# Performance work log

Hardware: AMD Instinct MI355X
Metric: run time of the kernel (lower is better)

Reference implementation:

```python
import jax, jax.numpy as jnp
import numpy as np
import math

D_K = 64

def setup_inputs() -> dict:
    key = jax.random.key(0)
    k1, k2, k3, k4 = jax.random.split(key, 4)
    BH, S, dk = 32, 2048, D_K
    q = jax.random.normal(k1, (BH, S, dk), dtype=jnp.float32)
    k = jax.random.normal(k2, (BH, S, dk), dtype=jnp.float32)
    v = jax.random.normal(k3, (BH, S, dk), dtype=jnp.float32)
    mask = jax.random.uniform(k4, (BH, S, S), dtype=jnp.float32)
    return {"q": q, "k": k, "v": v, "mask": mask}

def reference(q, k, v, mask):
    # scores: [BH, S, S]
    scores = jnp.einsum('bqd,bkd->bqk', q, k) * (1.0 / math.sqrt(D_K))
    masked = scores * mask  # multiplicative mask before softmax
    attn = jax.nn.softmax(masked, axis=-1)
    return jnp.einsum('bqk,bkd->bqd', attn, v)
```

## Files before the change

### kernel.cpp

```cpp
#include <hip/hip_runtime.h>
#include <hip/hip_bf16.h>

#define BH    32
#define SEQ   2048
#define DK    64
#define QBLK  256
#define KBLK  64
#define NIT   (SEQ / KBLK)
#define KSTR  72

typedef short  short8  __attribute__((ext_vector_type(8)));
typedef float  f32x4   __attribute__((ext_vector_type(4)));
typedef float  float4v __attribute__((ext_vector_type(4)));
typedef unsigned short ushort4v __attribute__((ext_vector_type(4)));

__device__ __forceinline__ unsigned short f2bf(float f) {
    unsigned int u = __builtin_bit_cast(unsigned int, f);
    u += 0x7FFFu + ((u >> 16) & 1u);
    return (unsigned short)(u >> 16);
}

#if __has_builtin(__builtin_amdgcn_exp2f)
#define EXP2F(x) __builtin_amdgcn_exp2f(x)
#else
#define EXP2F(x) exp2f(x)
#endif

__global__ __launch_bounds__(1024, 4)
void sdpa_kernel(const float* __restrict__ Q, const float* __restrict__ K,
                 const float* __restrict__ V, const float* __restrict__ M,
                 float* __restrict__ O)
{
    __shared__ unsigned short sK [2][KBLK][KSTR];
    __shared__ unsigned short sVt[2][DK][KSTR];
    __shared__ unsigned short sP [16][16][KSTR];

    const int tid  = threadIdx.x;
    const int wave = tid >> 6;
    const int lane = tid & 63;
    const int g    = lane >> 4;
    const int li   = lane & 15;

    const int b  = blockIdx.x;
    const int qb = blockIdx.y * QBLK;

    const float* Kb = K + (size_t)b * SEQ * DK;
    const float* Vb = V + (size_t)b * SEQ * DK;

    const float QSC = 0.125f * 1.44269504f;
    short8 aq[2];
    {
        const size_t qoff = ((size_t)b * SEQ + (qb + wave * 16 + li)) * DK;
        #pragma unroll
        for (int kk = 0; kk < 2; ++kk) {
            const float* qp = Q + qoff + kk * 32 + g * 8;
            float4v q0 = *(const float4v*)(qp);
            float4v q1 = *(const float4v*)(qp + 4);
            #pragma unroll
            for (int i = 0; i < 4; ++i) {
                aq[kk][i]     = (short)f2bf(q0[i] * QSC);
                aq[kk][i + 4] = (short)f2bf(q1[i] * QSC);
            }
        }
    }

    const int sr = tid >> 4;
    const int sc = (tid & 15) * 4;
    const int vd = tid & 63;
    const int vk = (tid >> 6) * 4;

    const float* kp = Kb + (size_t)sr * DK + sc;
    const float* vp = Vb + (size_t)vk * DK + vd;
    const float* mbase = M + ((size_t)b * SEQ + (qb + wave * 16 + g * 4)) * SEQ + li;

    float4v kreg = *(const float4v*)kp;
    float vreg0 = vp[0 * DK], vreg1 = vp[1 * DK], vreg2 = vp[2 * DK], vreg3 = vp[3 * DK];
    {
        ushort4v pk;
        pk[0] = f2bf(kreg[0]); pk[1] = f2bf(kreg[1]);
        pk[2] = f2bf(kreg[2]); pk[3] = f2bf(kreg[3]);
        *(ushort4v*)(&sK[0][sr][sc]) = pk;
        ushort4v pv_;
        pv_[0] = f2bf(vreg0); pv_[1] = f2bf(vreg1);
        pv_[2] = f2bf(vreg2); pv_[3] = f2bf(vreg3);
        *(ushort4v*)(&sVt[0][vd][vk]) = pv_;
    }
    kp += KBLK * DK;  vp += KBLK * DK;
    kreg = *(const float4v*)kp;
    vreg0 = vp[0 * DK]; vreg1 = vp[1 * DK]; vreg2 = vp[2 * DK]; vreg3 = vp[3 * DK];

    float mkA[4][4], mkB[4][4];
    #pragma unroll
    for (int r = 0; r < 4; ++r) {
        #pragma unroll
        for (int t = 0; t < 4; ++t)
            mkA[r][t] = mbase[(size_t)r * SEQ + t * 16];
    }

    __syncthreads();

    f32x4 oacc[4] = {};
    float lsum[4] = {0.f, 0.f, 0.f, 0.f};

#define SDPA_BODY(IT, CUR, MKC, MKN)                                          \
    {                                                                         \
        if ((IT) + 1 < NIT) {                                                 \
            const float* mp = mbase + (size_t)((IT) + 1) * KBLK;              \
            _Pragma("unroll")                                                 \
            for (int r = 0; r < 4; ++r) {                                     \
                _Pragma("unroll")                                             \
                for (int t = 0; t < 4; ++t)                                   \
                    MKN[r][t] = mp[(size_t)r * SEQ + t * 16];                 \
            }                                                                 \
            ushort4v pk;                                                      \
            pk[0] = f2bf(kreg[0]); pk[1] = f2bf(kreg[1]);                     \
            pk[2] = f2bf(kreg[2]); pk[3] = f2bf(kreg[3]);                     \
            *(ushort4v*)(&sK[(CUR) ^ 1][sr][sc]) = pk;                        \
            ushort4v pv_;                                                     \
            pv_[0] = f2bf(vreg0); pv_[1] = f2bf(vreg1);                       \
            pv_[2] = f2bf(vreg2); pv_[3] = f2bf(vreg3);                       \
            *(ushort4v*)(&sVt[(CUR) ^ 1][vd][vk]) = pv_;                      \
            if ((IT) + 2 < NIT) {                                             \
                kp += KBLK * DK;  vp += KBLK * DK;                            \
                kreg = *(const float4v*)kp;                                   \
                vreg0 = vp[0 * DK]; vreg1 = vp[1 * DK];                       \
                vreg2 = vp[2 * DK]; vreg3 = vp[3 * DK];                       \
            }                                                                 \
        }                                                                     \
        f32x4 sacc[4] = {};                                                   \
        _Pragma("unroll")                                                     \
        for (int t = 0; t < 4; ++t) {                                         \
            _Pragma("unroll")                                                 \
            for (int kk = 0; kk < 2; ++kk) {                                  \
                short8 bk = *(const short8*)(&sK[CUR][t * 16 + li][kk * 32 + g * 8]); \
                sacc[t] = __builtin_amdgcn_mfma_f32_16x16x32_bf16(aq[kk], bk, sacc[t], 0, 0, 0); \
            }                                                                 \
        }                                                                     \
        _Pragma("unroll")                                                     \
        for (int r = 0; r < 4; ++r) {                                         \
            float p0 = EXP2F(sacc[0][r] * MKC[r][0]);                         \
            float p1 = EXP2F(sacc[1][r] * MKC[r][1]);                         \
            float p2 = EXP2F(sacc[2][r] * MKC[r][2]);                         \
            float p3 = EXP2F(sacc[3][r] * MKC[r][3]);                         \
            lsum[r] += (p0 + p1) + (p2 + p3);                                 \
            sP[wave][g * 4 + r][0 * 16 + li] = f2bf(p0);                      \
            sP[wave][g * 4 + r][1 * 16 + li] = f2bf(p1);                      \
            sP[wave][g * 4 + r][2 * 16 + li] = f2bf(p2);                      \
            sP[wave][g * 4 + r][3 * 16 + li] = f2bf(p3);                      \
        }                                                                     \
        _Pragma("unroll")                                                     \
        for (int kk = 0; kk < 2; ++kk) {                                      \
            short8 pa = *(const short8*)(&sP[wave][li][kk * 32 + g * 8]);     \
            _Pragma("unroll")                                                 \
            for (int dt = 0; dt < 4; ++dt) {                                  \
                short8 bv = *(const short8*)(&sVt[CUR][dt * 16 + li][kk * 32 + g * 8]); \
                oacc[dt] = __builtin_amdgcn_mfma_f32_16x16x32_bf16(pa, bv, oacc[dt], 0, 0, 0); \
            }                                                                 \
        }                                                                     \
        __syncthreads();                                                      \
    }

    for (int it = 0; it < NIT; it += 2) {
        SDPA_BODY(it,     0, mkA, mkB)
        SDPA_BODY(it + 1, 1, mkB, mkA)
    }
#undef SDPA_BODY

    #pragma unroll
    for (int r = 0; r < 4; ++r) {
        float l = lsum[r];
        l += __shfl_xor(l, 1);
        l += __shfl_xor(l, 2);
        l += __shfl_xor(l, 4);
        l += __shfl_xor(l, 8);
        float inv = 1.0f / l;
        size_t orow = ((size_t)b * SEQ + (qb + wave * 16 + g * 4 + r)) * DK;
        #pragma unroll
        for (int dt = 0; dt < 4; ++dt)
            O[orow + dt * 16 + li] = oacc[dt][r] * inv;
    }
}

extern "C" void kernel_launch(void* const* d_in, const int* in_sizes, int n_in,
                              void* d_out, int out_size, void* d_ws, size_t ws_size,
                              hipStream_t stream) {
    const float* q = (const float*)d_in[0];
    const float* k = (const float*)d_in[1];
    const float* v = (const float*)d_in[2];
    const float* m = (const float*)d_in[3];
    float* o = (float*)d_out;

    dim3 grid(BH, SEQ / QBLK);
    sdpa_kernel<<<grid, dim3(1024), 0, stream>>>(q, k, v, m, o);
}
```

Baseline: 138.5 us.

## Pre-pack K and V to bf16 with transposed V in a workspace kernel

Adds a pack kernel that converts K to bf16 and writes V transposed in bf16 into the workspace. The attention kernel then loads ready bf16 tiles with vector loads instead of converting fp32 and gathering strided V elements on every block. This removes redundant per-block conversion and halves K/V read bytes, at the cost of an extra launch and a workspace round trip. It falls back to the original kernel if the workspace is too small.

```diff
diff --git a/kernel.cpp b/kernel.cpp
--- a/kernel.cpp
+++ b/kernel.cpp
@@ -13,6 +13,7 @@
 typedef float  f32x4   __attribute__((ext_vector_type(4)));
 typedef float  float4v __attribute__((ext_vector_type(4)));
 typedef unsigned short ushort4v __attribute__((ext_vector_type(4)));
+typedef unsigned short ushort8v __attribute__((ext_vector_type(8)));
 
 __device__ __forceinline__ unsigned short f2bf(float f) {
     unsigned int u = __builtin_bit_cast(unsigned int, f);
@@ -26,10 +27,198 @@
 #define EXP2F(x) exp2f(x)
 #endif
 
+__global__ __launch_bounds__(256)
+void pack_kv(const float* __restrict__ K, const float* __restrict__ V,
+             unsigned short* __restrict__ Kbf, unsigned short* __restrict__ Vt)
+{
+    __shared__ unsigned short tl[DK][KSTR];
+    const int b   = blockIdx.x;
+    const int kb  = blockIdx.y * KBLK;
+    const int tid = threadIdx.x;
+    const int r   = tid >> 2;
+    const int c   = (tid & 3) * 16;
+
+    {
+        const float* src = K + ((size_t)b * SEQ + kb + r) * DK + c;
+        float4v a0 = *(const float4v*)(src);
+        float4v a1 = *(const float4v*)(src + 4);
+        float4v a2 = *(const float4v*)(src + 8);
+        float4v a3 = *(const float4v*)(src + 12);
+        ushort8v o0, o1;
+        #pragma unroll
+        for (int e = 0; e < 4; ++e) {
+            o0[e] = f2bf(a0[e]); o0[e + 4] = f2bf(a1[e]);
+            o1[e] = f2bf(a2[e]); o1[e + 4] = f2bf(a3[e]);
+        }
+        unsigned short* dst = Kbf + ((size_t)b * SEQ + kb + r) * DK + c;
+        *(ushort8v*)(dst)     = o0;
+        *(ushort8v*)(dst + 8) = o1;
+    }
+    {
+        const float* src = V + ((size_t)b * SEQ + kb + r) * DK + c;
+        float4v a0 = *(const float4v*)(src);
+        float4v a1 = *(const float4v*)(src + 4);
+        float4v a2 = *(const float4v*)(src + 8);
+        float4v a3 = *(const float4v*)(src + 12);
+        #pragma unroll
+        for (int e = 0; e < 4; ++e) {
+            tl[c + e     ][r] = f2bf(a0[e]);
+            tl[c + e + 4 ][r] = f2bf(a1[e]);
+            tl[c + e + 8 ][r] = f2bf(a2[e]);
+            tl[c + e + 12][r] = f2bf(a3[e]);
+        }
+    }
+    __syncthreads();
+    {
+        const int d  = tid >> 2;
+        const int ch = (tid & 3) * 16;
+        ushort8v w0 = *(const ushort8v*)(&tl[d][ch]);
+        ushort8v w1 = *(const ushort8v*)(&tl[d][ch + 8]);
+        unsigned short* dst = Vt + ((size_t)b * DK + d) * SEQ + kb + ch;
+        *(ushort8v*)(dst)     = w0;
+        *(ushort8v*)(dst + 8) = w1;
+    }
+}
+
 __global__ __launch_bounds__(1024, 4)
-void sdpa_kernel(const float* __restrict__ Q, const float* __restrict__ K,
-                 const float* __restrict__ V, const float* __restrict__ M,
-                 float* __restrict__ O)
+void sdpa_bf16(const float* __restrict__ Q, const unsigned short* __restrict__ Kbf,
+               const unsigned short* __restrict__ Vt, const float* __restrict__ M,
+               float* __restrict__ O)
+{
+    __shared__ unsigned short sK [2][KBLK][KSTR];
+    __shared__ unsigned short sVt[2][DK][KSTR];
+    __shared__ unsigned short sP [16][16][KSTR];
+
+    const int tid  = threadIdx.x;
+    const int wave = tid >> 6;
+    const int lane = tid & 63;
+    const int g    = lane >> 4;
+    const int li   = lane & 15;
+
+    const int b  = blockIdx.x;
+    const int qb = blockIdx.y * QBLK;
+
+    const float QSC = 0.125f * 1.44269504f;
+    short8 aq[2];
+    {
+        const size_t qoff = ((size_t)b * SEQ + (qb + wave * 16 + li)) * DK;
+        #pragma unroll
+        for (int kk = 0; kk < 2; ++kk) {
+            const float* qp = Q + qoff + kk * 32 + g * 8;
+            float4v q0 = *(const float4v*)(qp);
+            float4v q1 = *(const float4v*)(qp + 4);
+            #pragma unroll
+            for (int i = 0; i < 4; ++i) {
+                aq[kk][i]     = (short)f2bf(q0[i] * QSC);
+                aq[kk][i + 4] = (short)f2bf(q1[i] * QSC);
+            }
+        }
+    }
+
+    const int sr = tid >> 4;
+    const int sc = (tid & 15) * 4;
+
+    const unsigned short* kp = Kbf + (size_t)b * SEQ * DK + (size_t)sr * DK + sc;
+    const unsigned short* vp = Vt  + (size_t)b * DK * SEQ + (size_t)sr * SEQ + sc;
+    const float* mbase = M + ((size_t)b * SEQ + (qb + wave * 16 + g * 4)) * SEQ + li;
+
+    ushort4v kreg = *(const ushort4v*)kp;
+    ushort4v vreg = *(const ushort4v*)vp;
+    *(ushort4v*)(&sK [0][sr][sc]) = kreg;
+    *(ushort4v*)(&sVt[0][sr][sc]) = vreg;
+    kp += KBLK * DK;  vp += KBLK;
+    kreg = *(const ushort4v*)kp;
+    vreg = *(const ushort4v*)vp;
+
+    float mkA[4][4], mkB[4][4];
+    #pragma unroll
+    for (int r = 0; r < 4; ++r) {
+        #pragma unroll
+        for (int t = 0; t < 4; ++t)
+            mkA[r][t] = mbase[(size_t)r * SEQ + t * 16];
+    }
+
+    __syncthreads();
+
+    f32x4 oacc[4] = {};
+    float lsum[4] = {0.f, 0.f, 0.f, 0.f};
+
+#define SDPA_BODY(IT, CUR, MKC, MKN)                                          \
+    {                                                                         \
+        if ((IT) + 1 < NIT) {                                                 \
+            const float* mp = mbase + (size_t)((IT) + 1) * KBLK;              \
+            _Pragma("unroll")                                                 \
+            for (int r = 0; r < 4; ++r) {                                     \
+                _Pragma("unroll")                                             \
+                for (int t = 0; t < 4; ++t)                                   \
+                    MKN[r][t] = mp[(size_t)r * SEQ + t * 16];                 \
+            }                                                                 \
+            *(ushort4v*)(&sK [(CUR) ^ 1][sr][sc]) = kreg;                     \
+            *(ushort4v*)(&sVt[(CUR) ^ 1][sr][sc]) = vreg;                     \
+            if ((IT) + 2 < NIT) {                                             \
+                kp += KBLK * DK;  vp += KBLK;                                 \
+                kreg = *(const ushort4v*)kp;                                  \
+                vreg = *(const ushort4v*)vp;                                  \
+            }                                                                 \
+        }                                                                     \
+        f32x4 sacc[4] = {};                                                   \
+        _Pragma("unroll")                                                     \
+        for (int t = 0; t < 4; ++t) {                                         \
+            _Pragma("unroll")                                                 \
+            for (int kk = 0; kk < 2; ++kk) {                                  \
+                short8 bk = *(const short8*)(&sK[CUR][t * 16 + li][kk * 32 + g * 8]); \
+                sacc[t] = __builtin_amdgcn_mfma_f32_16x16x32_bf16(aq[kk], bk, sacc[t], 0, 0, 0); \
+            }                                                                 \
+        }                                                                     \
+        _Pragma("unroll")                                                     \
+        for (int r = 0; r < 4; ++r) {                                         \
+            float p0 = EXP2F(sacc[0][r] * MKC[r][0]);                         \
+            float p1 = EXP2F(sacc[1][r] * MKC[r][1]);                         \
+            float p2 = EXP2F(sacc[2][r] * MKC[r][2]);                         \
+            float p3 = EXP2F(sacc[3][r] * MKC[r][3]);                         \
+            lsum[r] += (p0 + p1) + (p2 + p3);                                 \
+            sP[wave][g * 4 + r][0 * 16 + li] = f2bf(p0);                      \
+            sP[wave][g * 4 + r][1 * 16 + li] = f2bf(p1);                      \
+            sP[wave][g * 4 + r][2 * 16 + li] = f2bf(p2);                      \
+            sP[wave][g * 4 + r][3 * 16 + li] = f2bf(p3);                      \
+        }                                                                     \
+        _Pragma("unroll")                                                     \
+        for (int kk = 0; kk < 2; ++kk) {                                      \
+            short8 pa = *(const short8*)(&sP[wave][li][kk * 32 + g * 8]);     \
+            _Pragma("unroll")                                                 \
+            for (int dt = 0; dt < 4; ++dt) {                                  \
+                short8 bv = *(const short8*)(&sVt[CUR][dt * 16 + li][kk * 32 + g * 8]); \
+                oacc[dt] = __builtin_amdgcn_mfma_f32_16x16x32_bf16(pa, bv, oacc[dt], 0, 0, 0); \
+            }                                                                 \
+        }                                                                     \
+        __syncthreads();                                                      \
+    }
+
+    for (int it = 0; it < NIT; it += 2) {
+        SDPA_BODY(it,     0, mkA, mkB)
+        SDPA_BODY(it + 1, 1, mkB, mkA)
+    }
+#undef SDPA_BODY
+
+    #pragma unroll
+    for (int r = 0; r < 4; ++r) {
+        float l = lsum[r];
+        l += __shfl_xor(l, 1);
+        l += __shfl_xor(l, 2);
+        l += __shfl_xor(l, 4);
+        l += __shfl_xor(l, 8);
+        float inv = 1.0f / l;
+        size_t orow = ((size_t)b * SEQ + (qb + wave * 16 + g * 4 + r)) * DK;
+        #pragma unroll
+        for (int dt = 0; dt < 4; ++dt)
+            O[orow + dt * 16 + li] = oacc[dt][r] * inv;
+    }
+}
+
+__global__ __launch_bounds__(1024, 4)
+void sdpa_f32(const float* __restrict__ Q, const float* __restrict__ K,
+              const float* __restrict__ V, const float* __restrict__ M,
+              float* __restrict__ O)
 {
     __shared__ unsigned short sK [2][KBLK][KSTR];
     __shared__ unsigned short sVt[2][DK][KSTR];
@@ -190,6 +379,15 @@
     const float* m = (const float*)d_in[3];
     float* o = (float*)d_out;
 
-    dim3 grid(BH, SEQ / QBLK);
-    sdpa_kernel<<<grid, dim3(1024), 0, stream>>>(q, k, v, m, o);
-}
+    const size_t kv_elems = (size_t)BH * SEQ * DK;
+    const size_t need     = kv_elems * 2 * sizeof(unsigned short);
+
+    if (ws_size >= need) {
+        unsigned short* Kbf = (unsigned short*)d_ws;
+        unsigned short* Vt  = Kbf + kv_elems;
+        pack_kv<<<dim3(BH, SEQ / KBLK), dim3(256), 0, stream>>>(k, v, Kbf, Vt);
+        sdpa_bf16<<<dim3(BH, SEQ / QBLK), dim3(1024), 0, stream>>>(q, Kbf, Vt, m, o);
+    } else {
+        sdpa_f32<<<dim3(BH, SEQ / QBLK), dim3(1024), 0, stream>>>(q, k, v, m, o);
+    }
+}
```

Result: slower. 157.8 us (+13.9%).
